# Kernel tuning notes

Measured on AMD Instinct MI355X. Metric: run time of the kernel, lower is better.

## Reference

```python
import jax, jax.numpy as jnp
import numpy as np

N, T, L = 4, 2048, 2048
DQIN, DFEAT, DQK, DV = 32, 34, 64, 64  # modality feat=34 -> V input = 34-2 = 32, K input = last col


def _sorted_timeline(k, shape):
    return jnp.sort(jax.random.uniform(k, shape, jnp.float32) * 100.0, axis=-1)


def setup_inputs() -> dict:
    key = jax.random.key(0)
    ks = jax.random.split(key, 32)
    inp = {}
    inp["ref_data"] = jax.random.normal(ks[0], (N, 1, T, DQIN), jnp.float32)
    inp["ref_t"] = _sorted_timeline(ks[1], (N, 1, T))
    inp["m1_data"] = jax.random.normal(ks[2], (N, 1, L, DFEAT), jnp.float32)
    inp["m1_t"] = _sorted_timeline(ks[3], (N, 1, L))
    inp["m2_data"] = jax.random.normal(ks[4], (N, 1, L, DFEAT), jnp.float32)
    inp["m2_t"] = _sorted_timeline(ks[5], (N, 1, L))
    inp["m3_data"] = jax.random.normal(ks[6], (N, 1, L, DFEAT), jnp.float32)
    inp["m3_t"] = _sorted_timeline(ks[7], (N, 1, L))
    # shared W_Q (bias=False): d_q_in -> d_qk
    inp["Wq"] = jax.random.normal(ks[8], (DQIN, DQK), jnp.float32) / np.sqrt(DQIN)
    # per-modality params: W_K: 1 -> d_qk (with bias), W_V: (DFEAT-2) -> d_v (with bias), log-temperature
    for i, m in enumerate(["1", "2", "3"]):
        b = 9 + 4 * i
        inp["Wk" + m] = jax.random.normal(ks[b], (1, DQK), jnp.float32)
        inp["bk" + m] = jax.random.normal(ks[b + 1], (DQK,), jnp.float32) * 0.02
        inp["Wv" + m] = jax.random.normal(ks[b + 2], (DFEAT - 2, DV), jnp.float32) / np.sqrt(DFEAT - 2)
        inp["bv" + m] = jax.random.normal(ks[b + 3], (DV,), jnp.float32) * 0.02
        inp["log_tau" + m] = jnp.zeros((), jnp.float32)  # log(init_tau=1)
    return inp


def _unimodal(Q, ref_t, data, t, Wk, bk, Wv, bv, log_tau):
    # K path: last feature column through linear, then feature_map_k = [1, -x]
    Kr = data[..., -1:] @ Wk + bk                                   # (N,1,L,DQK)
    K = jnp.concatenate([jnp.ones(Kr.shape[:-1] + (1,), Kr.dtype), -Kr], axis=-1)  # (N,1,L,DQK+1)
    V = data[..., :-2] @ Wv + bv                                    # (N,1,L,DV)
    tau = jnp.exp(log_tau)
    # gaussian weight: -(Q.K)^2 / tau
    S = -jnp.square(jnp.einsum('nhtc,nhlc->nhtl', Q, K)) / tau       # (N,1,T,L)
    mask = (ref_t[..., :, None] >= t[..., None, :]).astype(S.dtype)  # (N,1,T,L)
    A = jax.nn.softmax(S * mask, axis=-1) * mask
    return jnp.einsum('nhtl,nhlc->nhtc', A, V)                       # (N,1,T,DV)


def reference(ref_data, ref_t, m1_data, m1_t, m2_data, m2_t, m3_data, m3_t,
              Wq, Wk1, bk1, Wv1, bv1, log_tau1, Wk2, bk2, Wv2, bv2, log_tau2,
              Wk3, bk3, Wv3, bv3, log_tau3):
    # compute_Q (qk_type='time'): Q = add_one(W_Q(ref_data)) -> append ones column
    Qr = jnp.einsum('nhtd,dk->nhtk', ref_data, Wq)
    Q = jnp.concatenate([Qr, jnp.ones(Qr.shape[:-1] + (1,), Qr.dtype)], axis=-1)  # (N,1,T,DQK+1)
    y1 = _unimodal(Q, ref_t, m1_data, m1_t, Wk1, bk1, Wv1, bv1, log_tau1)
    y2 = _unimodal(Q, ref_t, m2_data, m2_t, Wk2, bk2, Wv2, bv2, log_tau2)
    y3 = _unimodal(Q, ref_t, m3_data, m3_t, Wk3, bk3, Wv3, bv3, log_tau3)
    # original returns dict {m1: y1, m2: y2, m3: y3}; stacked here (3,N,1,T,DV)
    return jnp.stack([y1, y2, y3], axis=0)
```

## Files before the change

### kernel.cpp

```cpp
#include <hip/hip_runtime.h>

namespace {

typedef unsigned int uint;
typedef unsigned short ushort_t;
typedef __attribute__((ext_vector_type(8))) short bf16x8;
typedef __attribute__((ext_vector_type(4))) float f32x4;

constexpr int N = 4, T = 2048, L = 2048;
constexpr int DQIN = 32, DQK = 64;

constexpr int VI_SZ = 3 * N * 64 * L;
constexpr int X_SZ = 3 * N * L;
constexpr int A_SZ = 3 * N * T;

union PK8 { int i[4]; bf16x8 s; };

__global__ __launch_bounds__(256) void mm_prep(
    const float* __restrict__ ref_data, const float* __restrict__ ref_t,
    const float* __restrict__ d1, const float* __restrict__ t1,
    const float* __restrict__ d2, const float* __restrict__ t2,
    const float* __restrict__ d3, const float* __restrict__ t3,
    const float* __restrict__ Wq,
    const float* __restrict__ Wk1, const float* __restrict__ bk1,
    const float* __restrict__ Wv1, const float* __restrict__ bv1, const float* __restrict__ lt1,
    const float* __restrict__ Wk2, const float* __restrict__ bk2,
    const float* __restrict__ Wv2, const float* __restrict__ bv2, const float* __restrict__ lt2,
    const float* __restrict__ Wk3, const float* __restrict__ bk3,
    const float* __restrict__ Wv3, const float* __restrict__ bv3, const float* __restrict__ lt3,
    float* __restrict__ Aq, float* __restrict__ Gq, int* __restrict__ Cq,
    ushort_t* __restrict__ VI, float* __restrict__ X) {
  const int b = blockIdx.x;
  const int tid = threadIdx.x;

  if (b < 32) {
    const int idx = b * 256 + tid;
    __shared__ float sWq[DQIN * DQK];
    __shared__ float sWk[3][DQK];
    __shared__ float sbk[3][DQK];
    for (int i = tid; i < DQIN * DQK; i += 256) sWq[i] = Wq[i];
    if (tid < DQK) {
      sWk[0][tid] = Wk1[tid]; sbk[0][tid] = bk1[tid];
      sWk[1][tid] = Wk2[tid]; sbk[1][tid] = bk2[tid];
      sWk[2][tid] = Wk3[tid]; sbk[2][tid] = bk3[tid];
    }
    __syncthreads();
    float x[DQIN];
    const float* rp = ref_data + idx * DQIN;
#pragma unroll
    for (int i = 0; i < DQIN; i++) x[i] = rp[i];
    float qr[DQK];
#pragma unroll
    for (int j = 0; j < DQK; j += 4) {
      float4 acc4 = make_float4(0.f, 0.f, 0.f, 0.f);
#pragma unroll
      for (int i = 0; i < DQIN; i++) {
        const float4 w = *(const float4*)&sWq[i * DQK + j];
        acc4.x = fmaf(x[i], w.x, acc4.x);
        acc4.y = fmaf(x[i], w.y, acc4.y);
        acc4.z = fmaf(x[i], w.z, acc4.z);
        acc4.w = fmaf(x[i], w.w, acc4.w);
      }
      qr[j] = acc4.x; qr[j + 1] = acc4.y; qr[j + 2] = acc4.z; qr[j + 3] = acc4.w;
    }
    const float* lts[3] = {lt1, lt2, lt3};
#pragma unroll
    for (int m = 0; m < 3; m++) {
      const float rs = __expf(-0.5f * lts[m][0]);
      float g = 0.f, h = 0.f;
#pragma unroll
      for (int j = 1; j < DQK; j++) {
        g = fmaf(qr[j], sWk[m][j - 1], g);
        h = fmaf(qr[j], sbk[m][j - 1], h);
      }
      g += sWk[m][DQK - 1];
      h += sbk[m][DQK - 1];
      Aq[m * (N * T) + idx] = (qr[0] - h) * rs;
      Gq[m * (N * T) + idx] = g * rs;
    }
  } else if (b < 128) {
    const int sidx = (b - 32) * 256 + tid;
    const int m = sidx >> 13;
    const int nt = sidx & 8191;
    const int n = nt >> 11;
    const float rt = ref_t[nt];
    const float* tml = ((m == 0) ? t1 : (m == 1 ? t2 : t3)) + n * L;
    int lo = 0, hi = L;
    while (lo < hi) {
      const int mid = (lo + hi) >> 1;
      if (tml[mid] <= rt) lo = mid + 1; else hi = mid;
    }
    Cq[m * 8192 + nt] = lo;
  } else {
    const int vb = b - 128;
    const int mn = vb >> 7;
    const int m = mn >> 2, n = mn & 3;
    const int lseg = (vb & 127) * 16;
    const float* dm = (m == 0) ? d1 : (m == 1 ? d2 : d3);
    const float* Wv = (m == 0) ? Wv1 : (m == 1 ? Wv2 : Wv3);
    const float* bv = (m == 0) ? bv1 : (m == 1 ? bv2 : bv3);
    const int cdim = tid & 63;
    const int qq = tid >> 6;
    const int l0 = lseg + qq * 4;

    float Wc[32];
#pragma unroll
    for (int i = 0; i < 32; i++) Wc[i] = Wv[i * 64 + cdim];
    const float bvc = bv[cdim];

    uint hi16[4], lo16[4];
#pragma unroll
    for (int k = 0; k < 4; k++) {
      const float* dp = dm + (size_t)(n * L + l0 + k) * 34;
      float acc = bvc;
#pragma unroll
      for (int i = 0; i < 32; i += 2) {
        const float2 d2 = *(const float2*)&dp[i];
        acc = fmaf(d2.x, Wc[i], acc);
        acc = fmaf(d2.y, Wc[i + 1], acc);
      }
      uint u = __float_as_uint(acc);
      uint h = (u + 0x7fffu + ((u >> 16) & 1u)) & 0xffff0000u;
      float res = acc - __uint_as_float(h);
      uint ul = __float_as_uint(res);
      uint hl = (ul + 0x7fffu + ((ul >> 16) & 1u)) >> 16;
      hi16[k] = h >> 16;
      lo16[k] = hl;
    }
    const int pkh0 = (int)(hi16[0] | (hi16[1] << 16));
    const int pkh1 = (int)(hi16[2] | (hi16[3] << 16));
    const int pkl0 = (int)(lo16[0] | (lo16[1] << 16));
    const int pkl1 = (int)(lo16[2] | (lo16[3] << 16));
    ushort_t* dst = VI + (size_t)(mn * 64 + cdim) * (2 * L) +
                    (l0 >> 3) * 16 + ((l0 >> 2) & 1) * 4;
    *(int2*)dst = make_int2(pkh0, pkh1);
    *(int2*)(dst + 8) = make_int2(pkl0, pkl1);

    if (tid < 16) {
      const int l = lseg + tid;
      X[mn * L + l] = dm[(size_t)(n * L + l) * 34 + 33];
    }
  }
}

__device__ inline void stage_chunk(ushort_t* dstbuf, const ushort_t* VIb, int ch,
                                   int w, int lane) {
#pragma unroll
  for (int i = 0; i < 8; i++) {
    const int n = (w * 8 + i) * 64 + lane;
    const int d = n >> 4;
    const int s = n & 15;
    const int u = (s - d) & 15;
    const ushort_t* src = VIb + (size_t)d * 4096 + ch * 128 + u * 8;
    __builtin_amdgcn_global_load_lds(
        (const __attribute__((address_space(1))) void*)src,
        (__attribute__((address_space(3))) void*)(dstbuf + n * 8),
        16, 0, 0);
  }
}

__global__ __launch_bounds__(128, 2) void mm_attn_main(
    const ushort_t* __restrict__ VI, const float* __restrict__ X,
    const float* __restrict__ Aq, const float* __restrict__ Gq, const int* __restrict__ Cq,
    float* __restrict__ out) {
  __shared__ ushort_t sbuf[2][8192];
  __shared__ float sx[2048];

  const int b = blockIdx.x;
  const int mn = b % 12;
  const int rg = 127 - (b / 12);

  const int tid = threadIdx.x;
  const int lane = tid & 63;
  const int w = tid >> 6;
  const int q = lane >> 4;
  const int m16 = lane & 15;

  const int tbase = mn * T + rg * 16;

  const int c = Cq[tbase + m16];
  const int cmax = __shfl(c, 15, 64);
  const int cmin = __shfl(c, 0, 64);
  const int nch = (cmax + 63) >> 6;

  const float a = Aq[tbase + m16];
  const float g = Gq[tbase + m16];

  f32x4 acc[4];
#pragma unroll
  for (int i = 0; i < 4; i++) acc[i] = (f32x4){0.f, 0.f, 0.f, 0.f};
  float z = 0.f;

  const ushort_t* VIb = VI + (size_t)(mn * 64) * 4096;
  const float* xg = X + mn * L;

  int oh[2][2], ol[2][2];
#pragma unroll
  for (int hh = 0; hh < 2; hh++) {
#pragma unroll
    for (int ct = 0; ct < 2; ct++) {
      const int d = hh * 32 + ct * 16 + m16;
      const int u0 = (w * 4 + q) * 2;
      oh[hh][ct] = d * 128 + (((u0 + 0) + d) & 15) * 8;
      ol[hh][ct] = d * 128 + (((u0 + 1) + d) & 15) * 8;
    }
  }

#pragma unroll
  for (int i = 0; i < 4; i++) {
    const float* src = xg + (i * 128 + tid) * 4;
    __builtin_amdgcn_global_load_lds(
        (const __attribute__((address_space(1))) void*)src,
        (__attribute__((address_space(3))) void*)(sx + (i * 128 + tid) * 4),
        16, 0, 0);
  }
  if (nch > 0) stage_chunk(sbuf[0], VIb, 0, w, lane);

  for (int ch = 0; ch < nch; ch++) {
    if (ch + 1 < nch) {
      stage_chunk(sbuf[(ch + 1) & 1], VIb, ch + 1, w, lane);
      asm volatile("s_waitcnt vmcnt(8)" ::: "memory");
    } else {
      asm volatile("s_waitcnt vmcnt(0)" ::: "memory");
    }
    asm volatile("" ::: "memory");
    __builtin_amdgcn_s_barrier();
    asm volatile("" ::: "memory");

    const int kbase = (ch << 6) + w * 32;
    if (kbase < cmax) {
      const int k0 = kbase + q * 8;
      const float4 xa = *(const float4*)&sx[k0];
      const float4 xb = *(const float4*)&sx[k0 + 4];
      const float xs[8] = {xa.x, xa.y, xa.z, xa.w, xb.x, xb.y, xb.z, xb.w};
      float wv[8];
      if (kbase + 32 <= cmin) {
#pragma unroll
        for (int jj = 0; jj < 8; jj++) {
          const float d = fmaf(-g, xs[jj], a);
          wv[jj] = __expf(-d * d);
          z += wv[jj];
        }
      } else {
#pragma unroll
        for (int jj = 0; jj < 8; jj++) {
          const float d = fmaf(-g, xs[jj], a);
          const float e = __expf(-d * d);
          wv[jj] = (k0 + jj < c) ? e : 0.f;
          z += wv[jj];
        }
      }
      PK8 ph, pl;
#pragma unroll
      for (int p2 = 0; p2 < 4; p2++) {
        const uint u0 = __float_as_uint(wv[2 * p2]);
        const uint u1 = __float_as_uint(wv[2 * p2 + 1]);
        const uint h0 = u0 & 0xffff0000u, h1 = u1 & 0xffff0000u;
        const float l0f = wv[2 * p2] - __uint_as_float(h0);
        const float l1f = wv[2 * p2 + 1] - __uint_as_float(h1);
        ph.i[p2] = (int)((h0 >> 16) | h1);
        pl.i[p2] = (int)((__float_as_uint(l0f) >> 16) | (__float_as_uint(l1f) & 0xffff0000u));
      }
      const bf16x8 ahi = ph.s, alo = pl.s;
      const ushort_t* buf = sbuf[ch & 1];
#pragma unroll
      for (int hh = 0; hh < 2; hh++) {
#pragma unroll
        for (int ct = 0; ct < 2; ct++) {
          const bf16x8 bh = *(const bf16x8*)(buf + oh[hh][ct]);
          const bf16x8 bl = *(const bf16x8*)(buf + ol[hh][ct]);
          acc[hh * 2 + ct] =
              __builtin_amdgcn_mfma_f32_16x16x32_bf16(ahi, bh, acc[hh * 2 + ct], 0, 0, 0);
          acc[hh * 2 + ct] =
              __builtin_amdgcn_mfma_f32_16x16x32_bf16(ahi, bl, acc[hh * 2 + ct], 0, 0, 0);
          acc[hh * 2 + ct] =
              __builtin_amdgcn_mfma_f32_16x16x32_bf16(alo, bh, acc[hh * 2 + ct], 0, 0, 0);
        }
      }
    }

    asm volatile("" ::: "memory");
    __builtin_amdgcn_s_barrier();
    asm volatile("" ::: "memory");
  }

  z += __shfl_xor(z, 16, 64);
  z += __shfl_xor(z, 32, 64);

  float* sc = (float*)sbuf;
  const int ow = w ^ 1;
#pragma unroll
  for (int p = 0; p < 2; p++)
    *(f32x4*)&sc[((w * 2 + p) * 64 + lane) * 4] = acc[ow * 2 + p];
  sc[1024 + w * 64 + lane] = z;
  __syncthreads();
  const float zt = z + sc[1024 + ow * 64 + lane];
  f32x4 r[2];
#pragma unroll
  for (int p = 0; p < 2; p++)
    r[p] = acc[w * 2 + p] + *(const f32x4*)&sc[((ow * 2 + p) * 64 + lane) * 4];

#pragma unroll
  for (int rr = 0; rr < 4; rr++) {
    const int row = q * 4 + rr;
    const float zr = __shfl(zt, row, 64);
    const int cr = __shfl(c, row, 64);
    const float inv = 1.0f / (zr + (float)(L - cr));
#pragma unroll
    for (int p = 0; p < 2; p++) {
      out[(size_t)(tbase + row) * 64 + w * 32 + p * 16 + m16] = r[p][rr] * inv;
    }
  }
}

}

extern "C" void kernel_launch(void* const* d_in, const int* in_sizes, int n_in,
                              void* d_out, int out_size, void* d_ws, size_t ws_size,
                              hipStream_t stream) {
  const float* ref_data = (const float*)d_in[0];
  const float* ref_t = (const float*)d_in[1];
  const float* m1_data = (const float*)d_in[2];
  const float* m1_t = (const float*)d_in[3];
  const float* m2_data = (const float*)d_in[4];
  const float* m2_t = (const float*)d_in[5];
  const float* m3_data = (const float*)d_in[6];
  const float* m3_t = (const float*)d_in[7];
  const float* Wq = (const float*)d_in[8];
  const float* Wk1 = (const float*)d_in[9];
  const float* bk1 = (const float*)d_in[10];
  const float* Wv1 = (const float*)d_in[11];
  const float* bv1 = (const float*)d_in[12];
  const float* lt1 = (const float*)d_in[13];
  const float* Wk2 = (const float*)d_in[14];
  const float* bk2 = (const float*)d_in[15];
  const float* Wv2 = (const float*)d_in[16];
  const float* bv2 = (const float*)d_in[17];
  const float* lt2 = (const float*)d_in[18];
  const float* Wk3 = (const float*)d_in[19];
  const float* bk3 = (const float*)d_in[20];
  const float* Wv3 = (const float*)d_in[21];
  const float* bv3 = (const float*)d_in[22];
  const float* lt3 = (const float*)d_in[23];

  float* ws = (float*)d_ws;
  ushort_t* VI = (ushort_t*)ws;
  float* Xw = ws + VI_SZ;
  float* Aq = Xw + X_SZ;
  float* Gq = Aq + A_SZ;
  int* Cq = (int*)(Gq + A_SZ);

  mm_prep<<<dim3(1664), dim3(256), 0, stream>>>(
      ref_data, ref_t, m1_data, m1_t, m2_data, m2_t, m3_data, m3_t, Wq,
      Wk1, bk1, Wv1, bv1, lt1, Wk2, bk2, Wv2, bv2, lt2, Wk3, bk3, Wv3, bv3, lt3,
      Aq, Gq, Cq, VI, Xw);
  mm_attn_main<<<dim3(12 * 128), dim3(128), 0, stream>>>(
      VI, Xw, Aq, Gq, Cq, (float*)d_out);
}
```

Baseline: 147.6 us.

## Pre-swizzle V into MFMA fragment order and load directly from global

```diff
diff --git a/kernel.cpp b/kernel.cpp
--- a/kernel.cpp
+++ b/kernel.cpp
@@ -115,9 +115,9 @@
       float acc = bvc;
 #pragma unroll
       for (int i = 0; i < 32; i += 2) {
-        const float2 d2 = *(const float2*)&dp[i];
-        acc = fmaf(d2.x, Wc[i], acc);
-        acc = fmaf(d2.y, Wc[i + 1], acc);
+        const float2 dd = *(const float2*)&dp[i];
+        acc = fmaf(dd.x, Wc[i], acc);
+        acc = fmaf(dd.y, Wc[i + 1], acc);
       }
       uint u = __float_as_uint(acc);
       uint h = (u + 0x7fffu + ((u >> 16) & 1u)) & 0xffff0000u;
@@ -131,10 +131,14 @@
     const int pkh1 = (int)(hi16[2] | (hi16[3] << 16));
     const int pkl0 = (int)(lo16[0] | (lo16[1] << 16));
     const int pkl1 = (int)(lo16[2] | (lo16[3] << 16));
-    ushort_t* dst = VI + (size_t)(mn * 64 + cdim) * (2 * L) +
-                    (l0 >> 3) * 16 + ((l0 >> 2) & 1) * 4;
+
+    const int hh = cdim >> 5, ct = (cdim >> 4) & 1, m16f = cdim & 15;
+    const int ch = l0 >> 6, wf = (l0 >> 5) & 1, qf = (l0 >> 3) & 3, half = (l0 >> 2) & 1;
+    const int lanef = qf * 16 + m16f;
+    ushort_t* dst = VI + (size_t)mn * 262144 + (size_t)ch * 8192 + wf * 4096 +
+                    (hh * 2 + ct) * 1024 + lanef * 8 + half * 4;
     *(int2*)dst = make_int2(pkh0, pkh1);
-    *(int2*)(dst + 8) = make_int2(pkl0, pkl1);
+    *(int2*)(dst + 512) = make_int2(pkl0, pkl1);
 
     if (tid < 16) {
       const int l = lseg + tid;
@@ -143,28 +147,11 @@
   }
 }
 
-__device__ inline void stage_chunk(ushort_t* dstbuf, const ushort_t* VIb, int ch,
-                                   int w, int lane) {
-#pragma unroll
-  for (int i = 0; i < 8; i++) {
-    const int n = (w * 8 + i) * 64 + lane;
-    const int d = n >> 4;
-    const int s = n & 15;
-    const int u = (s - d) & 15;
-    const ushort_t* src = VIb + (size_t)d * 4096 + ch * 128 + u * 8;
-    __builtin_amdgcn_global_load_lds(
-        (const __attribute__((address_space(1))) void*)src,
-        (__attribute__((address_space(3))) void*)(dstbuf + n * 8),
-        16, 0, 0);
-  }
-}
-
-__global__ __launch_bounds__(128, 2) void mm_attn_main(
+__global__ __launch_bounds__(128, 4) void mm_attn_main(
     const ushort_t* __restrict__ VI, const float* __restrict__ X,
     const float* __restrict__ Aq, const float* __restrict__ Gq, const int* __restrict__ Cq,
     float* __restrict__ out) {
-  __shared__ ushort_t sbuf[2][8192];
-  __shared__ float sx[2048];
+  __shared__ float sc[1152];
 
   const int b = blockIdx.x;
   const int mn = b % 12;
@@ -181,7 +168,6 @@
   const int c = Cq[tbase + m16];
   const int cmax = __shfl(c, 15, 64);
   const int cmin = __shfl(c, 0, 64);
-  const int nch = (cmax + 63) >> 6;
 
   const float a = Aq[tbase + m16];
   const float g = Gq[tbase + m16];
@@ -191,103 +177,84 @@
   for (int i = 0; i < 4; i++) acc[i] = (f32x4){0.f, 0.f, 0.f, 0.f};
   float z = 0.f;
 
-  const ushort_t* VIb = VI + (size_t)(mn * 64) * 4096;
   const float* xg = X + mn * L;
 
-  int oh[2][2], ol[2][2];
-#pragma unroll
-  for (int hh = 0; hh < 2; hh++) {
-#pragma unroll
-    for (int ct = 0; ct < 2; ct++) {
-      const int d = hh * 32 + ct * 16 + m16;
-      const int u0 = (w * 4 + q) * 2;
-      oh[hh][ct] = d * 128 + (((u0 + 0) + d) & 15) * 8;
-      ol[hh][ct] = d * 128 + (((u0 + 1) + d) & 15) * 8;
-    }
+  const ushort_t* pb[4];
+#pragma unroll
+  for (int hh = 0; hh < 2; hh++)
+#pragma unroll
+    for (int ct = 0; ct < 2; ct++)
+      pb[hh * 2 + ct] = VI + (size_t)mn * 262144 + w * 4096 +
+                        (hh * 2 + ct) * 1024 + lane * 8;
+
+  const int nchw = (cmax > w * 32) ? ((cmax - w * 32 + 63) >> 6) : 0;
+
+  float4 xa, xb;
+  if (nchw > 0) {
+    const int k0 = w * 32 + q * 8;
+    xa = *(const float4*)&xg[k0];
+    xb = *(const float4*)&xg[k0 + 4];
   }
 
-#pragma unroll
-  for (int i = 0; i < 4; i++) {
-    const float* src = xg + (i * 128 + tid) * 4;
-    __builtin_amdgcn_global_load_lds(
-        (const __attribute__((address_space(1))) void*)src,
-        (__attribute__((address_space(3))) void*)(sx + (i * 128 + tid) * 4),
-        16, 0, 0);
-  }
-  if (nch > 0) stage_chunk(sbuf[0], VIb, 0, w, lane);
-
-  for (int ch = 0; ch < nch; ch++) {
-    if (ch + 1 < nch) {
-      stage_chunk(sbuf[(ch + 1) & 1], VIb, ch + 1, w, lane);
-      asm volatile("s_waitcnt vmcnt(8)" ::: "memory");
+  for (int ch = 0; ch < nchw; ch++) {
+    const int kbase = (ch << 6) + w * 32;
+    const int k0 = kbase + q * 8;
+    const float4 cxa = xa, cxb = xb;
+    if (ch + 1 < nchw) {
+      xa = *(const float4*)&xg[k0 + 64];
+      xb = *(const float4*)&xg[k0 + 68];
+    }
+    const float xs[8] = {cxa.x, cxa.y, cxa.z, cxa.w, cxb.x, cxb.y, cxb.z, cxb.w};
+    float wv[8];
+    if (kbase + 32 <= cmin) {
+#pragma unroll
+      for (int jj = 0; jj < 8; jj++) {
+        const float d = fmaf(-g, xs[jj], a);
+        wv[jj] = __expf(-d * d);
+        z += wv[jj];
+      }
     } else {
-      asm volatile("s_waitcnt vmcnt(0)" ::: "memory");
-    }
-    asm volatile("" ::: "memory");
-    __builtin_amdgcn_s_barrier();
-    asm volatile("" ::: "memory");
-
-    const int kbase = (ch << 6) + w * 32;
-    if (kbase < cmax) {
-      const int k0 = kbase + q * 8;
-      const float4 xa = *(const float4*)&sx[k0];
-      const float4 xb = *(const float4*)&sx[k0 + 4];
-      const float xs[8] = {xa.x, xa.y, xa.z, xa.w, xb.x, xb.y, xb.z, xb.w};
-      float wv[8];
-      if (kbase + 32 <= cmin) {
-#pragma unroll
-        for (int jj = 0; jj < 8; jj++) {
-          const float d = fmaf(-g, xs[jj], a);
-          wv[jj] = __expf(-d * d);
-          z += wv[jj];
-        }
-      } else {
-#pragma unroll
-        for (int jj = 0; jj < 8; jj++) {
-          const float d = fmaf(-g, xs[jj], a);
-          const float e = __expf(-d * d);
-          wv[jj] = (k0 + jj < c) ? e : 0.f;
-          z += wv[jj];
-        }
-      }
-      PK8 ph, pl;
-#pragma unroll
-      for (int p2 = 0; p2 < 4; p2++) {
-        const uint u0 = __float_as_uint(wv[2 * p2]);
-        const uint u1 = __float_as_uint(wv[2 * p2 + 1]);
-        const uint h0 = u0 & 0xffff0000u, h1 = u1 & 0xffff0000u;
-        const float l0f = wv[2 * p2] - __uint_as_float(h0);
-        const float l1f = wv[2 * p2 + 1] - __uint_as_float(h1);
-        ph.i[p2] = (int)((h0 >> 16) | h1);
-        pl.i[p2] = (int)((__float_as_uint(l0f) >> 16) | (__float_as_uint(l1f) & 0xffff0000u));
-      }
-      const bf16x8 ahi = ph.s, alo = pl.s;
-      const ushort_t* buf = sbuf[ch & 1];
-#pragma unroll
-      for (int hh = 0; hh < 2; hh++) {
-#pragma unroll
-        for (int ct = 0; ct < 2; ct++) {
-          const bf16x8 bh = *(const bf16x8*)(buf + oh[hh][ct]);
-          const bf16x8 bl = *(const bf16x8*)(buf + ol[hh][ct]);
-          acc[hh * 2 + ct] =
-              __builtin_amdgcn_mfma_f32_16x16x32_bf16(ahi, bh, acc[hh * 2 + ct], 0, 0, 0);
-          acc[hh * 2 + ct] =
-              __builtin_amdgcn_mfma_f32_16x16x32_bf16(ahi, bl, acc[hh * 2 + ct], 0, 0, 0);
-          acc[hh * 2 + ct] =
-              __builtin_amdgcn_mfma_f32_16x16x32_bf16(alo, bh, acc[hh * 2 + ct], 0, 0, 0);
-        }
-      }
-    }
-
-    asm volatile("" ::: "memory");
-    __builtin_amdgcn_s_barrier();
-    asm volatile("" ::: "memory");
+#pragma unroll
+      for (int jj = 0; jj < 8; jj++) {
+        const float d = fmaf(-g, xs[jj], a);
+        const float e = __expf(-d * d);
+        wv[jj] = (k0 + jj < c) ? e : 0.f;
+        z += wv[jj];
+      }
+    }
+    PK8 ph, pl;
+#pragma unroll
+    for (int p2 = 0; p2 < 4; p2++) {
+      const uint u0 = __float_as_uint(wv[2 * p2]);
+      const uint u1 = __float_as_uint(wv[2 * p2 + 1]);
+      const uint h0 = u0 & 0xffff0000u, h1 = u1 & 0xffff0000u;
+      const float l0f = wv[2 * p2] - __uint_as_float(h0);
+      const float l1f = wv[2 * p2 + 1] - __uint_as_float(h1);
+      ph.i[p2] = (int)((h0 >> 16) | h1);
+      pl.i[p2] = (int)((__float_as_uint(l0f) >> 16) | (__float_as_uint(l1f) & 0xffff0000u));
+    }
+    const bf16x8 ahi = ph.s, alo = pl.s;
+    const size_t choff = (size_t)ch * 8192;
+#pragma unroll
+    for (int hh = 0; hh < 2; hh++) {
+#pragma unroll
+      for (int ct = 0; ct < 2; ct++) {
+        const ushort_t* p = pb[hh * 2 + ct] + choff;
+        const bf16x8 bh = *(const bf16x8*)p;
+        const bf16x8 bl = *(const bf16x8*)(p + 512);
+        acc[hh * 2 + ct] =
+            __builtin_amdgcn_mfma_f32_16x16x32_bf16(ahi, bh, acc[hh * 2 + ct], 0, 0, 0);
+        acc[hh * 2 + ct] =
+            __builtin_amdgcn_mfma_f32_16x16x32_bf16(ahi, bl, acc[hh * 2 + ct], 0, 0, 0);
+        acc[hh * 2 + ct] =
+            __builtin_amdgcn_mfma_f32_16x16x32_bf16(alo, bh, acc[hh * 2 + ct], 0, 0, 0);
+      }
+    }
   }
 
   z += __shfl_xor(z, 16, 64);
   z += __shfl_xor(z, 32, 64);
 
-  float* sc = (float*)sbuf;
   const int ow = w ^ 1;
 #pragma unroll
   for (int p = 0; p < 2; p++)
```

New measurement: 146.0 us. No clear change (-1.1%).
